# Optimization experiments

Measured on AMD Instinct MI355X. Metric: run time of the kernel, lower is better.

## Reference

```python
import jax, jax.numpy as jnp
import numpy as np

MAX_LEN = 128
VOCAB = 32000
SENTINEL = 2**30  # larger than any valid token id; pushes masked slots to the end after sort


def setup_inputs() -> dict:
    key = jax.random.key(0)
    k1, k2, k3, k4 = jax.random.split(key, 4)
    B, L = 262144, MAX_LEN
    input_ids = jax.random.randint(k1, (B, L), 0, VOCAB, dtype=jnp.int32)
    attention_mask = jax.random.randint(k2, (B, L), 0, 2, dtype=jnp.int32)
    # MLP params: Linear(3,32) -> ReLU -> Linear(32,32) -> ReLU
    W1 = jax.random.normal(k3, (3, 32), dtype=jnp.float32) * (1.0 / np.sqrt(3.0))
    b1 = jnp.zeros((32,), dtype=jnp.float32)
    W2 = jax.random.normal(k4, (32, 32), dtype=jnp.float32) * (1.0 / np.sqrt(32.0))
    b2 = jnp.zeros((32,), dtype=jnp.float32)
    return {"input_ids": input_ids, "attention_mask": attention_mask,
            "W1": W1, "b1": b1, "W2": W2, "b2": b2}


def _symbolic_feats(input_ids, attention_mask):
    # Batched replacement of the per-row torch.unique loop:
    # sort masked tokens per row, count boundaries between distinct values.
    mask = attention_mask.astype(bool)
    seq_len = jnp.sum(mask, axis=1)  # [B]
    ids_m = jnp.where(mask, input_ids, SENTINEL)  # masked-out slots -> sentinel
    s = jnp.sort(ids_m, axis=1)  # valid tokens first (ids < SENTINEL)
    valid = s < SENTINEL
    first = jnp.ones((s.shape[0], 1), dtype=bool)
    new_val = jnp.concatenate([first, s[:, 1:] != s[:, :-1]], axis=1)
    uniq = jnp.sum(valid & new_val, axis=1)  # [B] unique count among valid tokens
    seq_f = seq_len.astype(jnp.float32)
    uniq_f = uniq.astype(jnp.float32)
    uniq_ratio = jnp.where(seq_len > 0, uniq_f / jnp.maximum(seq_f, 1.0), 0.0)
    feats = jnp.stack([seq_f / MAX_LEN, uniq_f / MAX_LEN, uniq_ratio], axis=1)  # [B,3]
    return feats


def reference(input_ids, attention_mask, W1, b1, W2, b2):
    feats = _symbolic_feats(input_ids, attention_mask)  # [B,3]
    h = jax.nn.relu(feats @ W1 + b1)
    out = jax.nn.relu(h @ W2 + b2)
    return out
```

## Files before the change

### kernel.cpp

```cpp
#include <hip/hip_runtime.h>

#define ROW_LEN 128
#define NPAIR (129 * 129)

__global__ __launch_bounds__(256) void mlp_table_kernel(
    const float* __restrict__ W1, const float* __restrict__ b1,
    const float* __restrict__ W2, const float* __restrict__ b2,
    float* __restrict__ table)
{
    const int tid = blockIdx.x * 256 + threadIdx.x;
    if (tid >= NPAIR * 32) return;
    const int p = tid >> 5;
    const int j = tid & 31;
    const int seq  = p / 129;
    const int uniq = p % 129;
    const float f0 = (float)seq  * (1.0f / 128.0f);
    const float f1 = (float)uniq * (1.0f / 128.0f);
    const float f2 = (seq > 0) ? ((float)uniq / (float)seq) : 0.0f;

    float acc = b2[j];
    #pragma unroll
    for (int jj = 0; jj < 32; ++jj) {
        float h = b1[jj];
        h = fmaf(f0, W1[jj],      h);
        h = fmaf(f1, W1[32 + jj], h);
        h = fmaf(f2, W1[64 + jj], h);
        h = fmaxf(h, 0.0f);
        acc = fmaf(h, W2[jj * 32 + j], acc);
    }
    table[tid] = fmaxf(acc, 0.0f);
}

__global__ __launch_bounds__(256) void rows_kernel(
    const int* __restrict__ ids, const int* __restrict__ amask,
    const float* __restrict__ table, float* __restrict__ out, int B)
{
    __shared__ unsigned bm[8][1024];

    const int wave = threadIdx.x >> 6;
    const int lane = threadIdx.x & 63;
    const int half = lane >> 5;
    const long pair = (long)blockIdx.x * 4 + wave;
    if (pair * 2 >= B) return;

    const long v = pair * 64 + lane;
    const int4 id4 = ((const int4*)ids)[v];
    const int4 mk4 = ((const int4*)amask)[v];

    uint4* z = (uint4*)bm[wave * 2];
    #pragma unroll
    for (int i = 0; i < 8; ++i) z[lane + i * 64] = make_uint4(0u, 0u, 0u, 0u);

    unsigned* mybm = bm[wave * 2 + half];

    int n0 = 0, n1 = 0, n2 = 0, n3 = 0;
    if (mk4.x != 0) {
        const unsigned t = (unsigned)id4.x, m = 1u << (t & 31u);
        n0 = ((atomicOr(&mybm[t >> 5], m) & m) == 0u);
    }
    if (mk4.y != 0) {
        const unsigned t = (unsigned)id4.y, m = 1u << (t & 31u);
        n1 = ((atomicOr(&mybm[t >> 5], m) & m) == 0u);
    }
    if (mk4.z != 0) {
        const unsigned t = (unsigned)id4.z, m = 1u << (t & 31u);
        n2 = ((atomicOr(&mybm[t >> 5], m) & m) == 0u);
    }
    if (mk4.w != 0) {
        const unsigned t = (unsigned)id4.w, m = 1u << (t & 31u);
        n3 = ((atomicOr(&mybm[t >> 5], m) & m) == 0u);
    }

    const unsigned long long s0 = __ballot(mk4.x != 0);
    const unsigned long long s1 = __ballot(mk4.y != 0);
    const unsigned long long s2 = __ballot(mk4.z != 0);
    const unsigned long long s3 = __ballot(mk4.w != 0);
    const unsigned long long u0 = __ballot(n0 != 0);
    const unsigned long long u1 = __ballot(n1 != 0);
    const unsigned long long u2 = __ballot(n2 != 0);
    const unsigned long long u3 = __ballot(n3 != 0);

    const int sh = lane & 32;
    const int seq  = __popc((unsigned)(s0 >> sh)) + __popc((unsigned)(s1 >> sh))
                   + __popc((unsigned)(s2 >> sh)) + __popc((unsigned)(s3 >> sh));
    const int uniq = __popc((unsigned)(u0 >> sh)) + __popc((unsigned)(u1 >> sh))
                   + __popc((unsigned)(u2 >> sh)) + __popc((unsigned)(u3 >> sh));

    const int p = seq * 129 + uniq;
    out[pair * 64 + lane] = table[p * 32 + (lane & 31)];
}

extern "C" void kernel_launch(void* const* d_in, const int* in_sizes, int n_in,
                              void* d_out, int out_size, void* d_ws, size_t ws_size,
                              hipStream_t stream) {
    const int*   ids   = (const int*)d_in[0];
    const int*   amask = (const int*)d_in[1];
    const float* W1    = (const float*)d_in[2];
    const float* b1    = (const float*)d_in[3];
    const float* W2    = (const float*)d_in[4];
    const float* b2    = (const float*)d_in[5];
    float* out   = (float*)d_out;
    float* table = (float*)d_ws;

    const int B = in_sizes[0] / ROW_LEN;

    const int tblThreads = NPAIR * 32;
    mlp_table_kernel<<<(tblThreads + 255) / 256, 256, 0, stream>>>(W1, b1, W2, b2, table);

    rows_kernel<<<(B + 7) / 8, 256, 0, stream>>>(ids, amask, table, out, B);
}
```

Baseline: 281.1 us.

## Make rows kernel persistent with register prefetch and sparse bitmap clearing

Replaces the one-pair-per-wave launch with a fixed grid of 1280 blocks that grid-stride over row pairs. Each iteration prefetches the next pair's ids and mask into registers while the current pair is processed. The shared-memory bitmap is cleared once, then only the words touched by the current row are reset instead of re-zeroing 4 KB per row. This removes per-block launch and zeroing overhead and overlaps global loads with the atomics, at the cost of lower occupancy and reliance on the fixed grid size to cover the GPU.

```diff
diff --git a/kernel.cpp b/kernel.cpp
--- a/kernel.cpp
+++ b/kernel.cpp
@@ -33,61 +33,83 @@
 
 __global__ __launch_bounds__(256) void rows_kernel(
     const int* __restrict__ ids, const int* __restrict__ amask,
-    const float* __restrict__ table, float* __restrict__ out, int B)
+    const float* __restrict__ table, float* __restrict__ out, long npairs)
 {
     __shared__ unsigned bm[8][1024];
 
     const int wave = threadIdx.x >> 6;
     const int lane = threadIdx.x & 63;
     const int half = lane >> 5;
-    const long pair = (long)blockIdx.x * 4 + wave;
-    if (pair * 2 >= B) return;
-
-    const long v = pair * 64 + lane;
-    const int4 id4 = ((const int4*)ids)[v];
-    const int4 mk4 = ((const int4*)amask)[v];
+    const int sh   = lane & 32;
 
     uint4* z = (uint4*)bm[wave * 2];
     #pragma unroll
     for (int i = 0; i < 8; ++i) z[lane + i * 64] = make_uint4(0u, 0u, 0u, 0u);
-
     unsigned* mybm = bm[wave * 2 + half];
 
-    int n0 = 0, n1 = 0, n2 = 0, n3 = 0;
-    if (mk4.x != 0) {
-        const unsigned t = (unsigned)id4.x, m = 1u << (t & 31u);
-        n0 = ((atomicOr(&mybm[t >> 5], m) & m) == 0u);
-    }
-    if (mk4.y != 0) {
-        const unsigned t = (unsigned)id4.y, m = 1u << (t & 31u);
-        n1 = ((atomicOr(&mybm[t >> 5], m) & m) == 0u);
-    }
-    if (mk4.z != 0) {
-        const unsigned t = (unsigned)id4.z, m = 1u << (t & 31u);
-        n2 = ((atomicOr(&mybm[t >> 5], m) & m) == 0u);
-    }
-    if (mk4.w != 0) {
-        const unsigned t = (unsigned)id4.w, m = 1u << (t & 31u);
-        n3 = ((atomicOr(&mybm[t >> 5], m) & m) == 0u);
+    long pair = (long)blockIdx.x * 4 + wave;
+    const long stride = (long)gridDim.x * 4;
+    if (pair >= npairs) return;
+
+    int4 id4, mk4;
+    {
+        const long v = pair * 64 + lane;
+        id4 = ((const int4*)ids)[v];
+        mk4 = ((const int4*)amask)[v];
     }
 
-    const unsigned long long s0 = __ballot(mk4.x != 0);
-    const unsigned long long s1 = __ballot(mk4.y != 0);
-    const unsigned long long s2 = __ballot(mk4.z != 0);
-    const unsigned long long s3 = __ballot(mk4.w != 0);
-    const unsigned long long u0 = __ballot(n0 != 0);
-    const unsigned long long u1 = __ballot(n1 != 0);
-    const unsigned long long u2 = __ballot(n2 != 0);
-    const unsigned long long u3 = __ballot(n3 != 0);
+    for (; pair < npairs; pair += stride) {
+        const long nxt = pair + stride;
+        int4 id4n = make_int4(0, 0, 0, 0), mk4n = make_int4(0, 0, 0, 0);
+        if (nxt < npairs) {
+            const long vn = nxt * 64 + lane;
+            id4n = ((const int4*)ids)[vn];
+            mk4n = ((const int4*)amask)[vn];
+        }
 
-    const int sh = lane & 32;
-    const int seq  = __popc((unsigned)(s0 >> sh)) + __popc((unsigned)(s1 >> sh))
-                   + __popc((unsigned)(s2 >> sh)) + __popc((unsigned)(s3 >> sh));
-    const int uniq = __popc((unsigned)(u0 >> sh)) + __popc((unsigned)(u1 >> sh))
-                   + __popc((unsigned)(u2 >> sh)) + __popc((unsigned)(u3 >> sh));
+        int n0 = 0, n1 = 0, n2 = 0, n3 = 0;
+        if (mk4.x != 0) {
+            const unsigned t = (unsigned)id4.x, m = 1u << (t & 31u);
+            n0 = ((atomicOr(&mybm[t >> 5], m) & m) == 0u);
+        }
+        if (mk4.y != 0) {
+            const unsigned t = (unsigned)id4.y, m = 1u << (t & 31u);
+            n1 = ((atomicOr(&mybm[t >> 5], m) & m) == 0u);
+        }
+        if (mk4.z != 0) {
+            const unsigned t = (unsigned)id4.z, m = 1u << (t & 31u);
+            n2 = ((atomicOr(&mybm[t >> 5], m) & m) == 0u);
+        }
+        if (mk4.w != 0) {
+            const unsigned t = (unsigned)id4.w, m = 1u << (t & 31u);
+            n3 = ((atomicOr(&mybm[t >> 5], m) & m) == 0u);
+        }
 
-    const int p = seq * 129 + uniq;
-    out[pair * 64 + lane] = table[p * 32 + (lane & 31)];
+        const unsigned long long s0 = __ballot(mk4.x != 0);
+        const unsigned long long s1 = __ballot(mk4.y != 0);
+        const unsigned long long s2 = __ballot(mk4.z != 0);
+        const unsigned long long s3 = __ballot(mk4.w != 0);
+        const unsigned long long u0 = __ballot(n0 != 0);
+        const unsigned long long u1 = __ballot(n1 != 0);
+        const unsigned long long u2 = __ballot(n2 != 0);
+        const unsigned long long u3 = __ballot(n3 != 0);
+
+        const int seq  = __popc((unsigned)(s0 >> sh)) + __popc((unsigned)(s1 >> sh))
+                       + __popc((unsigned)(s2 >> sh)) + __popc((unsigned)(s3 >> sh));
+        const int uniq = __popc((unsigned)(u0 >> sh)) + __popc((unsigned)(u1 >> sh))
+                       + __popc((unsigned)(u2 >> sh)) + __popc((unsigned)(u3 >> sh));
+
+        if (mk4.x != 0) mybm[((unsigned)id4.x) >> 5] = 0u;
+        if (mk4.y != 0) mybm[((unsigned)id4.y) >> 5] = 0u;
+        if (mk4.z != 0) mybm[((unsigned)id4.z) >> 5] = 0u;
+        if (mk4.w != 0) mybm[((unsigned)id4.w) >> 5] = 0u;
+
+        const int p = seq * 129 + uniq;
+        out[pair * 64 + lane] = table[p * 32 + (lane & 31)];
+
+        id4 = id4n;
+        mk4 = mk4n;
+    }
 }
 
 extern "C" void kernel_launch(void* const* d_in, const int* in_sizes, int n_in,
@@ -103,9 +125,11 @@
     float* table = (float*)d_ws;
 
     const int B = in_sizes[0] / ROW_LEN;
+    const long npairs = B / 2;
 
     const int tblThreads = NPAIR * 32;
     mlp_table_kernel<<<(tblThreads + 255) / 256, 256, 0, stream>>>(W1, b1, W2, b2, table);
 
-    rows_kernel<<<(B + 7) / 8, 256, 0, stream>>>(ids, amask, table, out, B);
+    const int blocks = 1280;
+    rows_kernel<<<blocks, 256, 0, stream>>>(ids, amask, table, out, npairs);
 }
```

Result: slower. 311.6 us (+10.9%).
